# Kernel optimization log

Measured on AMD Instinct MI355X. Metric: run time of the kernel, lower is better.

## Reference

```python
import jax, jax.numpy as jnp
import numpy as np

V, E, NH, NL, FF, MAXLEN = 32000, 512, 8, 4, 2048, 80
B, L = 32, 80
EPS = 1e-5


def _ln(x, w, b):
    m = jnp.mean(x, axis=-1, keepdims=True)
    v = jnp.var(x, axis=-1, keepdims=True)
    return (x - m) / jnp.sqrt(v + EPS) * w + b


def _mha(q_in, kv_in, in_w, in_b, out_w, out_b, mask):
    # in_w: [3E, E] packed q/k/v like torch MultiheadAttention
    Bq, Lq, Em = q_in.shape
    Lk = kv_in.shape[1]
    hd = Em // NH
    q = q_in @ in_w[:Em].T + in_b[:Em]
    k = kv_in @ in_w[Em:2 * Em].T + in_b[Em:2 * Em]
    v = kv_in @ in_w[2 * Em:].T + in_b[2 * Em:]
    q = q.reshape(Bq, Lq, NH, hd).transpose(0, 2, 1, 3)
    k = k.reshape(Bq, Lk, NH, hd).transpose(0, 2, 1, 3)
    v = v.reshape(Bq, Lk, NH, hd).transpose(0, 2, 1, 3)
    s = jnp.einsum('bhqd,bhkd->bhqk', q, k) * (1.0 / float(np.sqrt(hd)))
    if mask is not None:
        s = s + mask
    a = jax.nn.softmax(s, axis=-1)
    o = jnp.einsum('bhqk,bhkd->bhqd', a, v).transpose(0, 2, 1, 3).reshape(Bq, Lq, Em)
    return o @ out_w.T + out_b


def _forward(caps, W_in, b_in, pos_emb, sa_in_w, sa_in_b, sa_out_w, sa_out_b,
             ca_in_w, ca_in_b, ca_out_w, ca_out_b, ff1_w, ff1_b, ff2_w, ff2_b,
             ln1_w, ln1_b, ln2_w, ln2_b, ln3_w, ln3_b, out_w, out_b):
    Bc, Lc = caps.shape
    # one-hot encode then dense Linear(vocab -> emb): semantically an embedding gather
    oh = jax.nn.one_hot(caps, V, dtype=jnp.float32)          # [B, L, V]
    x = oh @ W_in.T + b_in + pos_emb[:Lc][None]               # [B, L, E]
    mask = jnp.where(jnp.triu(jnp.ones((Lc, Lc), bool), 1), -jnp.inf, 0.0).astype(jnp.float32)
    mem = jnp.zeros((Bc, 1, E), jnp.float32)
    for i in range(NL):  # post-norm TransformerDecoderLayer (torch default, relu FFN)
        sa = _mha(x, x, sa_in_w[i], sa_in_b[i], sa_out_w[i], sa_out_b[i], mask)
        x = _ln(x + sa, ln1_w[i], ln1_b[i])
        ca = _mha(x, mem, ca_in_w[i], ca_in_b[i], ca_out_w[i], ca_out_b[i], None)
        x = _ln(x + ca, ln2_w[i], ln2_b[i])
        ff = jax.nn.relu(x @ ff1_w[i].T + ff1_b[i]) @ ff2_w[i].T + ff2_b[i]
        x = _ln(x + ff, ln3_w[i], ln3_b[i])
    return x @ out_w.T + out_b                                # [B, L, V]


def setup_inputs() -> dict:
    key = jax.random.key(0)
    ks = jax.random.split(key, 16)
    g = lambda k, shape, s=0.02: jax.random.normal(k, shape, jnp.float32) * s
    caps = jax.random.randint(ks[0], (B, L), 1, V)  # avoid pad_idx=0
    return {
        'caps': caps,
        'W_in': g(ks[1], (E, V)),
        'b_in': jnp.zeros((E,), jnp.float32),
        'pos_emb': g(ks[2], (MAXLEN, E)),
        'sa_in_w': g(ks[3], (NL, 3 * E, E)),
        'sa_in_b': jnp.zeros((NL, 3 * E), jnp.float32),
        'sa_out_w': g(ks[4], (NL, E, E)),
        'sa_out_b': jnp.zeros((NL, E), jnp.float32),
        'ca_in_w': g(ks[5], (NL, 3 * E, E)),
        'ca_in_b': jnp.zeros((NL, 3 * E), jnp.float32),
        'ca_out_w': g(ks[6], (NL, E, E)),
        'ca_out_b': jnp.zeros((NL, E), jnp.float32),
        'ff1_w': g(ks[7], (NL, FF, E)),
        'ff1_b': jnp.zeros((NL, FF), jnp.float32),
        'ff2_w': g(ks[8], (NL, E, FF)),
        'ff2_b': jnp.zeros((NL, E), jnp.float32),
        'ln1_w': jnp.ones((NL, E), jnp.float32),
        'ln1_b': jnp.zeros((NL, E), jnp.float32),
        'ln2_w': jnp.ones((NL, E), jnp.float32),
        'ln2_b': jnp.zeros((NL, E), jnp.float32),
        'ln3_w': jnp.ones((NL, E), jnp.float32),
        'ln3_b': jnp.zeros((NL, E), jnp.float32),
        'out_w': g(ks[9], (V, E)),
        'out_b': jnp.zeros((V,), jnp.float32),
    }


def reference(caps, W_in, b_in, pos_emb, sa_in_w, sa_in_b, sa_out_w, sa_out_b,
              ca_in_w, ca_in_b, ca_out_w, ca_out_b, ff1_w, ff1_b, ff2_w, ff2_b,
              ln1_w, ln1_b, ln2_w, ln2_b, ln3_w, ln3_b, out_w, out_b):
    return _forward(caps, W_in, b_in, pos_emb, sa_in_w, sa_in_b, sa_out_w, sa_out_b,
                    ca_in_w, ca_in_b, ca_out_w, ca_out_b, ff1_w, ff1_b, ff2_w, ff2_b,
                    ln1_w, ln1_b, ln2_w, ln2_b, ln3_w, ln3_b, out_w, out_b)
```

## Files before the change

kernel.cpp:

```cpp
#include <hip/hip_runtime.h>

typedef __attribute__((ext_vector_type(8))) short short8;
typedef __attribute__((ext_vector_type(4))) float floatx4;

__device__ __forceinline__ unsigned short f2bf(float f) {
  union { float f; unsigned int u; } un; un.f = f;
  unsigned int r = un.u + 0x7FFFu + ((un.u >> 16) & 1u);
  return (unsigned short)(r >> 16);
}
__device__ __forceinline__ float bf2f(unsigned short h) {
  union { unsigned int u; float f; } un; un.u = ((unsigned int)h) << 16;
  return un.f;
}

__device__ __forceinline__ void async_ld16(const unsigned short* g, unsigned short* l) {
  __builtin_amdgcn_global_load_lds(
      (const __attribute__((address_space(1))) void*)g,
      (__attribute__((address_space(3))) void*)l, 16, 0, 0);
}

template<int OUT_BF16, int RELU>
__global__ __launch_bounds__(256, 2)
void gemm_bt(const unsigned short* __restrict__ A, const unsigned short* __restrict__ B,
             const float* __restrict__ bias, const float* __restrict__ res,
             void* __restrict__ Cout, int M, int N, int K) {
  __shared__ __align__(16) unsigned short sA[128 * 64];
  __shared__ __align__(16) unsigned short sB[128 * 64];
  const int tid  = threadIdx.x;
  const int lane = tid & 63;
  const int wave = tid >> 6;
  const int m0 = blockIdx.y * 128;
  const int n0 = blockIdx.x * 128;

  floatx4 acc[4][4];
#pragma unroll
  for (int i = 0; i < 4; i++)
#pragma unroll
    for (int j = 0; j < 4; j++) acc[i][j] = (floatx4){0.f, 0.f, 0.f, 0.f};

  int s_r[4], s_gc[4], s_lb[4];
#pragma unroll
  for (int it = 0; it < 4; it++) {
    int e = it * 2048 + tid * 8;
    int r = e >> 6;
    int cb = (e >> 3) & 7;
    s_r[it]  = r;
    s_gc[it] = (cb ^ (r & 7)) * 8;
    s_lb[it] = it * 2048 + wave * 512;
  }

  const int nkt = K >> 6;
  const int wm = (wave >> 1) * 64;
  const int wn = (wave & 1) * 64;
  const int fr = lane & 15;
  const int q  = lane >> 4;

  for (int kt = 0; kt < nkt; kt++) {
    const int k0 = kt << 6;
#pragma unroll
    for (int it = 0; it < 4; it++) {
      async_ld16(A + (size_t)(m0 + s_r[it]) * K + k0 + s_gc[it], &sA[s_lb[it]]);
      async_ld16(B + (size_t)(n0 + s_r[it]) * K + k0 + s_gc[it], &sB[s_lb[it]]);
    }
    __syncthreads();
#pragma unroll
    for (int kk = 0; kk < 64; kk += 32) {
      short8 af[4], bfr[4];
#pragma unroll
      for (int t = 0; t < 4; t++) {
        int ra = wm + t * 16 + fr;
        int cba = (kk >> 3) + q;
        af[t] = *(const short8*)&sA[ra * 64 + ((cba ^ (ra & 7)) * 8)];
        int rb = wn + t * 16 + fr;
        bfr[t] = *(const short8*)&sB[rb * 64 + ((cba ^ (rb & 7)) * 8)];
      }
#pragma unroll
      for (int i = 0; i < 4; i++)
#pragma unroll
        for (int j = 0; j < 4; j++)
          acc[i][j] = __builtin_amdgcn_mfma_f32_16x16x32_bf16(af[i], bfr[j], acc[i][j], 0, 0, 0);
    }
    __syncthreads();
  }

#pragma unroll
  for (int i = 0; i < 4; i++) {
#pragma unroll
    for (int j = 0; j < 4; j++) {
#pragma unroll
      for (int rg = 0; rg < 4; rg++) {
        int row = m0 + wm + i * 16 + q * 4 + rg;
        int col = n0 + wn + j * 16 + fr;
        float v = acc[i][j][rg];
        if (bias) v += bias[col];
        if (res)  v += res[(size_t)row * N + col];
        if (RELU) v = v > 0.f ? v : 0.f;
        if (OUT_BF16) ((unsigned short*)Cout)[(size_t)row * N + col] = f2bf(v);
        else          ((float*)Cout)[(size_t)row * N + col] = v;
      }
    }
  }
}

__global__ __launch_bounds__(512)
void embed_kernel(const int* __restrict__ caps, const float* __restrict__ W_in,
                  const float* __restrict__ b_in, const float* __restrict__ pos,
                  float* __restrict__ x, unsigned short* __restrict__ xbf) {
  int pidx = blockIdx.x;
  int l = pidx % 80;
  int tok = caps[pidx];
  int e = threadIdx.x;
  float v = W_in[(size_t)e * 32000 + tok] + b_in[e] + pos[l * 512 + e];
  x[(size_t)pidx * 512 + e] = v;
  xbf[(size_t)pidx * 512 + e] = f2bf(v);
}

__global__ __launch_bounds__(256)
void ln_kernel(const float* __restrict__ in, const float* __restrict__ addvec,
               const float* __restrict__ w, const float* __restrict__ b,
               float* __restrict__ xout, unsigned short* __restrict__ xbf) {
  int row = blockIdx.x * 4 + (threadIdx.x >> 6);
  int lane = threadIdx.x & 63;
  const float* p = in + (size_t)row * 512;
  float vals[8];
  float s = 0.f, s2 = 0.f;
#pragma unroll
  for (int j = 0; j < 8; j++) {
    float t = p[lane + j * 64];
    if (addvec) t += addvec[lane + j * 64];
    vals[j] = t; s += t; s2 += t * t;
  }
#pragma unroll
  for (int off = 32; off; off >>= 1) { s += __shfl_xor(s, off); s2 += __shfl_xor(s2, off); }
  float mean = s * (1.f / 512.f);
  float var = s2 * (1.f / 512.f) - mean * mean;
  float inv = rsqrtf(var + 1e-5f);
#pragma unroll
  for (int j = 0; j < 8; j++) {
    int c = lane + j * 64;
    float y = (vals[j] - mean) * inv * w[c] + b[c];
    xout[(size_t)row * 512 + c] = y;
    xbf[(size_t)row * 512 + c] = f2bf(y);
  }
}

__global__ __launch_bounds__(256)
void attn_kernel(const unsigned short* __restrict__ qkv, unsigned short* __restrict__ o) {
  __shared__ unsigned short sq[80][66], sk[80][66], sv[80][66];
  __shared__ float ss[80][81];
  const int tid = threadIdx.x;
  const int bb = blockIdx.x >> 3, hh = blockIdx.x & 7;
  const unsigned short* base = qkv + (size_t)bb * 80 * 1536 + hh * 64;
  for (int idx = tid; idx < 5120; idx += 256) {
    int r = idx >> 6, c = idx & 63;
    sq[r][c] = base[r * 1536 + c];
    sk[r][c] = base[r * 1536 + 512 + c];
    sv[r][c] = base[r * 1536 + 1024 + c];
  }
  __syncthreads();
  {
    const int ti = tid >> 4, tj = tid & 15;
    float acc[5][5];
#pragma unroll
    for (int a = 0; a < 5; a++)
#pragma unroll
      for (int b2 = 0; b2 < 5; b2++) acc[a][b2] = 0.f;
    for (int c = 0; c < 64; c++) {
      float qa[5], kb[5];
#pragma unroll
      for (int a = 0; a < 5; a++) qa[a] = bf2f(sq[ti + a * 16][c]);
#pragma unroll
      for (int b2 = 0; b2 < 5; b2++) kb[b2] = bf2f(sk[tj + b2 * 16][c]);
#pragma unroll
      for (int a = 0; a < 5; a++)
#pragma unroll
        for (int b2 = 0; b2 < 5; b2++) acc[a][b2] += qa[a] * kb[b2];
    }
#pragma unroll
    for (int a = 0; a < 5; a++)
#pragma unroll
      for (int b2 = 0; b2 < 5; b2++) {
        int i = ti + a * 16, j = tj + b2 * 16;
        ss[i][j] = (j <= i) ? acc[a][b2] * 0.125f : -1e30f;
      }
  }
  __syncthreads();
  if (tid < 80) {
    float mx = -1e30f;
    for (int j = 0; j < 80; j++) mx = fmaxf(mx, ss[tid][j]);
    float sum = 0.f;
    for (int j = 0; j < 80; j++) { float e2 = __expf(ss[tid][j] - mx); ss[tid][j] = e2; sum += e2; }
    float inv = 1.f / sum;
    for (int j = 0; j < 80; j++) ss[tid][j] *= inv;
  }
  __syncthreads();
  {
    const int ti = tid >> 4, td = tid & 15;
    float acc[5][4];
#pragma unroll
    for (int a = 0; a < 5; a++)
#pragma unroll
      for (int b2 = 0; b2 < 4; b2++) acc[a][b2] = 0.f;
    for (int j = 0; j < 80; j++) {
      float pa[5], vb[4];
#pragma unroll
      for (int a = 0; a < 5; a++) pa[a] = ss[ti + a * 16][j];
#pragma unroll
      for (int b2 = 0; b2 < 4; b2++) vb[b2] = bf2f(sv[j][td + b2 * 16]);
#pragma unroll
      for (int a = 0; a < 5; a++)
#pragma unroll
        for (int b2 = 0; b2 < 4; b2++) acc[a][b2] += pa[a] * vb[b2];
    }
#pragma unroll
    for (int a = 0; a < 5; a++)
#pragma unroll
      for (int b2 = 0; b2 < 4; b2++) {
        int i = ti + a * 16, d = td + b2 * 16;
        o[((size_t)bb * 80 + i) * 512 + hh * 64 + d] = f2bf(acc[a][b2]);
      }
  }
}

__global__ __launch_bounds__(256)
void cavec_kernel(const float* __restrict__ w, const float* __restrict__ inb,
                  const float* __restrict__ ob, float* __restrict__ out) {
  int e = blockIdx.x * 4 + (threadIdx.x >> 6);
  int lane = threadIdx.x & 63;
  const float* row = w + (size_t)e * 512;
  float s = 0.f;
#pragma unroll
  for (int j = 0; j < 8; j++) s += row[lane + j * 64] * inb[1024 + lane + j * 64];
#pragma unroll
  for (int off = 32; off; off >>= 1) s += __shfl_xor(s, off);
  if (lane == 0) out[e] = s + ob[e];
}

__global__ __launch_bounds__(256)
void convert_f2bf(const float* __restrict__ in, unsigned short* __restrict__ out, int n4) {
  int i = blockIdx.x * 256 + threadIdx.x;
  if (i < n4) {
    float4 v = ((const float4*)in)[i];
    ushort4 r;
    r.x = f2bf(v.x); r.y = f2bf(v.y); r.z = f2bf(v.z); r.w = f2bf(v.w);
    ((ushort4*)out)[i] = r;
  }
}

extern "C" void kernel_launch(void* const* d_in, const int* in_sizes, int n_in,
                              void* d_out, int out_size, void* d_ws, size_t ws_size,
                              hipStream_t stream) {
  const int*   caps     = (const int*)d_in[0];
  const float* W_in     = (const float*)d_in[1];
  const float* b_in     = (const float*)d_in[2];
  const float* pos_emb  = (const float*)d_in[3];
  const float* sa_in_w  = (const float*)d_in[4];
  const float* sa_in_b  = (const float*)d_in[5];
  const float* sa_out_w = (const float*)d_in[6];
  const float* sa_out_b = (const float*)d_in[7];
  const float* ca_in_b  = (const float*)d_in[9];
  const float* ca_out_w = (const float*)d_in[10];
  const float* ca_out_b = (const float*)d_in[11];
  const float* ff1_w    = (const float*)d_in[12];
  const float* ff1_b    = (const float*)d_in[13];
  const float* ff2_w    = (const float*)d_in[14];
  const float* ff2_b    = (const float*)d_in[15];
  const float* ln1_w    = (const float*)d_in[16];
  const float* ln1_b    = (const float*)d_in[17];
  const float* ln2_w    = (const float*)d_in[18];
  const float* ln2_b    = (const float*)d_in[19];
  const float* ln3_w    = (const float*)d_in[20];
  const float* ln3_b    = (const float*)d_in[21];
  const float* out_w    = (const float*)d_in[22];
  const float* out_b    = (const float*)d_in[23];

  char* ws = (char*)d_ws;
  size_t off = 0;
  auto alloc = [&](size_t bytes) {
    void* p = ws + off;
    off += (bytes + 255) & ~(size_t)255;
    return p;
  };
  unsigned short* w_sa_in  = (unsigned short*)alloc((size_t)4 * 1536 * 512 * 2);
  unsigned short* w_sa_out = (unsigned short*)alloc((size_t)4 * 512 * 512 * 2);
  unsigned short* w_ff1    = (unsigned short*)alloc((size_t)4 * 2048 * 512 * 2);
  unsigned short* w_ff2    = (unsigned short*)alloc((size_t)4 * 512 * 2048 * 2);
  unsigned short* w_out    = (unsigned short*)alloc((size_t)32000 * 512 * 2);
  float*          x        = (float*)alloc((size_t)2560 * 512 * 4);
  unsigned short* xbf      = (unsigned short*)alloc((size_t)2560 * 512 * 2);
  float*          t        = (float*)alloc((size_t)2560 * 512 * 4);
  unsigned short* qkv      = (unsigned short*)alloc((size_t)2560 * 1536 * 2);
  unsigned short* obf      = (unsigned short*)alloc((size_t)2560 * 512 * 2);
  unsigned short* hbf      = (unsigned short*)alloc((size_t)2560 * 2048 * 2);
  float*          cav      = (float*)alloc((size_t)512 * 4);

  convert_f2bf<<<(786432 + 255) / 256, 256, 0, stream>>>(sa_in_w, w_sa_in, 786432);
  convert_f2bf<<<(262144 + 255) / 256, 256, 0, stream>>>(sa_out_w, w_sa_out, 262144);
  convert_f2bf<<<(1048576 + 255) / 256, 256, 0, stream>>>(ff1_w, w_ff1, 1048576);
  convert_f2bf<<<(1048576 + 255) / 256, 256, 0, stream>>>(ff2_w, w_ff2, 1048576);
  convert_f2bf<<<(4096000 + 255) / 256, 256, 0, stream>>>(out_w, w_out, 4096000);

  embed_kernel<<<2560, 512, 0, stream>>>(caps, W_in, b_in, pos_emb, x, xbf);

  for (int i = 0; i < 4; i++) {
    gemm_bt<1, 0><<<dim3(12, 20), 256, 0, stream>>>(
        xbf, w_sa_in + (size_t)i * 1536 * 512, sa_in_b + i * 1536, nullptr,
        qkv, 2560, 1536, 512);
    attn_kernel<<<256, 256, 0, stream>>>(qkv, obf);
    gemm_bt<0, 0><<<dim3(4, 20), 256, 0, stream>>>(
        obf, w_sa_out + (size_t)i * 512 * 512, sa_out_b + i * 512, x,
        t, 2560, 512, 512);
    ln_kernel<<<640, 256, 0, stream>>>(t, nullptr, ln1_w + i * 512, ln1_b + i * 512, x, xbf);
    cavec_kernel<<<128, 256, 0, stream>>>(
        ca_out_w + (size_t)i * 512 * 512, ca_in_b + (size_t)i * 1536, ca_out_b + i * 512, cav);
    ln_kernel<<<640, 256, 0, stream>>>(x, cav, ln2_w + i * 512, ln2_b + i * 512, x, xbf);
    gemm_bt<1, 1><<<dim3(16, 20), 256, 0, stream>>>(
        xbf, w_ff1 + (size_t)i * 2048 * 512, ff1_b + i * 2048, nullptr,
        hbf, 2560, 2048, 512);
    gemm_bt<0, 0><<<dim3(4, 20), 256, 0, stream>>>(
        hbf, w_ff2 + (size_t)i * 512 * 2048, ff2_b + i * 512, x,
        t, 2560, 512, 2048);
    ln_kernel<<<640, 256, 0, stream>>>(t, nullptr, ln3_w + i * 512, ln3_b + i * 512, x, xbf);
  }

  gemm_bt<0, 0><<<dim3(250, 20), 256, 0, stream>>>(
      xbf, w_out, out_b, nullptr, (float*)d_out, 2560, 32000, 512);
}
```

Baseline: 1.288 ms.

## Double-buffer GEMM, templatize tiles, MFMA attention, fuse LN1/LN2, hoist cross-attn vector

The GEMM kernel now double-buffers its LDS tiles so the next K-slice's async loads overlap the current MFMAs, and it is templated on tile size. The N=512 GEMMs use 64x64 tiles for more blocks, and the grid is swapped so M varies fastest. Attention computes QK^T and PV with bf16 MFMA instead of scalar FMAs, with V transposed and P rounded to bf16. LN1 and LN2 are fused into one kernel, and the constant cross-attention vector is computed once for all layers before the loop. The costs are doubled LDS use and extra bf16 rounding of the attention probabilities.

```diff
diff --git a/kernel.cpp b/kernel.cpp
--- a/kernel.cpp
+++ b/kernel.cpp
@@ -19,74 +19,92 @@
       (__attribute__((address_space(3))) void*)l, 16, 0, 0);
 }
 
-template<int OUT_BF16, int RELU>
-__global__ __launch_bounds__(256, 2)
+template<int TM, int TN, int OUT_BF16, int RELU>
+__global__ __launch_bounds__(256, (TM == 64) ? 4 : 2)
 void gemm_bt(const unsigned short* __restrict__ A, const unsigned short* __restrict__ B,
              const float* __restrict__ bias, const float* __restrict__ res,
              void* __restrict__ Cout, int M, int N, int K) {
-  __shared__ __align__(16) unsigned short sA[128 * 64];
-  __shared__ __align__(16) unsigned short sB[128 * 64];
-  const int tid  = threadIdx.x;
+  constexpr int AELEM = TM * 64;
+  constexpr int BELEM = TN * 64;
+  constexpr int AIT = AELEM / 2048;
+  constexpr int BIT = BELEM / 2048;
+  constexpr int FM = TM / 32;
+  constexpr int FN = TN / 32;
+  __shared__ __align__(16) unsigned short sA[2][AELEM];
+  __shared__ __align__(16) unsigned short sB[2][BELEM];
+  const int tid = threadIdx.x;
   const int lane = tid & 63;
   const int wave = tid >> 6;
-  const int m0 = blockIdx.y * 128;
-  const int n0 = blockIdx.x * 128;
-
-  floatx4 acc[4][4];
-#pragma unroll
-  for (int i = 0; i < 4; i++)
-#pragma unroll
-    for (int j = 0; j < 4; j++) acc[i][j] = (floatx4){0.f, 0.f, 0.f, 0.f};
-
-  int s_r[4], s_gc[4], s_lb[4];
-#pragma unroll
-  for (int it = 0; it < 4; it++) {
+  const int m0 = blockIdx.x * TM;
+  const int n0 = blockIdx.y * TN;
+
+  int a_off[AIT], b_off[BIT], lb[AIT > BIT ? AIT : BIT];
+#pragma unroll
+  for (int it = 0; it < AIT; it++) {
     int e = it * 2048 + tid * 8;
-    int r = e >> 6;
-    int cb = (e >> 3) & 7;
-    s_r[it]  = r;
-    s_gc[it] = (cb ^ (r & 7)) * 8;
-    s_lb[it] = it * 2048 + wave * 512;
-  }
+    int r = e >> 6, cb = (e >> 3) & 7;
+    a_off[it] = (m0 + r) * K + ((cb ^ (r & 7)) * 8);
+    lb[it] = it * 2048 + wave * 512;
+  }
+#pragma unroll
+  for (int it = 0; it < BIT; it++) {
+    int e = it * 2048 + tid * 8;
+    int r = e >> 6, cb = (e >> 3) & 7;
+    b_off[it] = (n0 + r) * K + ((cb ^ (r & 7)) * 8);
+  }
+
+  floatx4 acc[FM][FN];
+#pragma unroll
+  for (int i = 0; i < FM; i++)
+#pragma unroll
+    for (int j = 0; j < FN; j++) acc[i][j] = (floatx4){0.f, 0.f, 0.f, 0.f};
 
   const int nkt = K >> 6;
-  const int wm = (wave >> 1) * 64;
-  const int wn = (wave & 1) * 64;
+  const int wm = (wave >> 1) * (TM / 2);
+  const int wn = (wave & 1) * (TN / 2);
   const int fr = lane & 15;
-  const int q  = lane >> 4;
-
+  const int q = lane >> 4;
+
+  auto stage = [&](int kt, int buf) {
+    const int k0 = kt << 6;
+#pragma unroll
+    for (int it = 0; it < AIT; it++) async_ld16(A + (size_t)a_off[it] + k0, &sA[buf][lb[it]]);
+#pragma unroll
+    for (int it = 0; it < BIT; it++) async_ld16(B + (size_t)b_off[it] + k0, &sB[buf][lb[it]]);
+  };
+
+  stage(0, 0);
   for (int kt = 0; kt < nkt; kt++) {
-    const int k0 = kt << 6;
-#pragma unroll
-    for (int it = 0; it < 4; it++) {
-      async_ld16(A + (size_t)(m0 + s_r[it]) * K + k0 + s_gc[it], &sA[s_lb[it]]);
-      async_ld16(B + (size_t)(n0 + s_r[it]) * K + k0 + s_gc[it], &sB[s_lb[it]]);
-    }
     __syncthreads();
+    if (kt + 1 < nkt) stage(kt + 1, (kt + 1) & 1);
+    const unsigned short* pA = sA[kt & 1];
+    const unsigned short* pB = sB[kt & 1];
 #pragma unroll
     for (int kk = 0; kk < 64; kk += 32) {
-      short8 af[4], bfr[4];
-#pragma unroll
-      for (int t = 0; t < 4; t++) {
+      short8 af[FM], bfr[FN];
+      const int cba = (kk >> 3) + q;
+#pragma unroll
+      for (int t = 0; t < FM; t++) {
         int ra = wm + t * 16 + fr;
-        int cba = (kk >> 3) + q;
-        af[t] = *(const short8*)&sA[ra * 64 + ((cba ^ (ra & 7)) * 8)];
+        af[t] = *(const short8*)&pA[ra * 64 + ((cba ^ (ra & 7)) * 8)];
+      }
+#pragma unroll
+      for (int t = 0; t < FN; t++) {
         int rb = wn + t * 16 + fr;
-        bfr[t] = *(const short8*)&sB[rb * 64 + ((cba ^ (rb & 7)) * 8)];
+        bfr[t] = *(const short8*)&pB[rb * 64 + ((cba ^ (rb & 7)) * 8)];
       }
 #pragma unroll
-      for (int i = 0; i < 4; i++)
-#pragma unroll
-        for (int j = 0; j < 4; j++)
+      for (int i = 0; i < FM; i++)
+#pragma unroll
+        for (int j = 0; j < FN; j++)
           acc[i][j] = __builtin_amdgcn_mfma_f32_16x16x32_bf16(af[i], bfr[j], acc[i][j], 0, 0, 0);
     }
-    __syncthreads();
-  }
-
-#pragma unroll
-  for (int i = 0; i < 4; i++) {
-#pragma unroll
-    for (int j = 0; j < 4; j++) {
+  }
+
+#pragma unroll
+  for (int i = 0; i < FM; i++) {
+#pragma unroll
+    for (int j = 0; j < FN; j++) {
 #pragma unroll
       for (int rg = 0; rg < 4; rg++) {
         int row = m0 + wm + i * 16 + q * 4 + rg;
@@ -116,9 +134,9 @@
 }
 
 __global__ __launch_bounds__(256)
-void ln_kernel(const float* __restrict__ in, const float* __restrict__ addvec,
-               const float* __restrict__ w, const float* __restrict__ b,
-               float* __restrict__ xout, unsigned short* __restrict__ xbf) {
+void ln_kernel(const float* __restrict__ in, const float* __restrict__ w,
+               const float* __restrict__ b, float* __restrict__ xout,
+               unsigned short* __restrict__ xbf) {
   int row = blockIdx.x * 4 + (threadIdx.x >> 6);
   int lane = threadIdx.x & 63;
   const float* p = in + (size_t)row * 512;
@@ -127,14 +145,12 @@
 #pragma unroll
   for (int j = 0; j < 8; j++) {
     float t = p[lane + j * 64];
-    if (addvec) t += addvec[lane + j * 64];
     vals[j] = t; s += t; s2 += t * t;
   }
 #pragma unroll
   for (int off = 32; off; off >>= 1) { s += __shfl_xor(s, off); s2 += __shfl_xor(s2, off); }
   float mean = s * (1.f / 512.f);
-  float var = s2 * (1.f / 512.f) - mean * mean;
-  float inv = rsqrtf(var + 1e-5f);
+  float inv = rsqrtf(s2 * (1.f / 512.f) - mean * mean + 1e-5f);
 #pragma unroll
   for (int j = 0; j < 8; j++) {
     int c = lane + j * 64;
@@ -145,95 +161,131 @@
 }
 
 __global__ __launch_bounds__(256)
+void ln2x_kernel(const float* __restrict__ in, const float* __restrict__ cav,
+                 const float* __restrict__ w1, const float* __restrict__ b1,
+                 const float* __restrict__ w2, const float* __restrict__ b2,
+                 float* __restrict__ xout, unsigned short* __restrict__ xbf) {
+  int row = blockIdx.x * 4 + (threadIdx.x >> 6);
+  int lane = threadIdx.x & 63;
+  const float* p = in + (size_t)row * 512;
+  float vals[8];
+  float s = 0.f, s2 = 0.f;
+#pragma unroll
+  for (int j = 0; j < 8; j++) {
+    float t = p[lane + j * 64];
+    vals[j] = t; s += t; s2 += t * t;
+  }
+#pragma unroll
+  for (int off = 32; off; off >>= 1) { s += __shfl_xor(s, off); s2 += __shfl_xor(s2, off); }
+  float mean = s * (1.f / 512.f);
+  float inv = rsqrtf(s2 * (1.f / 512.f) - mean * mean + 1e-5f);
+  float s_b = 0.f, s2_b = 0.f;
+#pragma unroll
+  for (int j = 0; j < 8; j++) {
+    int c = lane + j * 64;
+    float y = (vals[j] - mean) * inv * w1[c] + b1[c] + cav[c];
+    vals[j] = y; s_b += y; s2_b += y * y;
+  }
+#pragma unroll
+  for (int off = 32; off; off >>= 1) { s_b += __shfl_xor(s_b, off); s2_b += __shfl_xor(s2_b, off); }
+  float mean2 = s_b * (1.f / 512.f);
+  float inv2 = rsqrtf(s2_b * (1.f / 512.f) - mean2 * mean2 + 1e-5f);
+#pragma unroll
+  for (int j = 0; j < 8; j++) {
+    int c = lane + j * 64;
+    float y = (vals[j] - mean2) * inv2 * w2[c] + b2[c];
+    xout[(size_t)row * 512 + c] = y;
+    xbf[(size_t)row * 512 + c] = f2bf(y);
+  }
+}
+
+__global__ __launch_bounds__(256)
 void attn_kernel(const unsigned short* __restrict__ qkv, unsigned short* __restrict__ o) {
-  __shared__ unsigned short sq[80][66], sk[80][66], sv[80][66];
-  __shared__ float ss[80][81];
+  __shared__ __align__(16) unsigned short sq[80][72];
+  __shared__ __align__(16) unsigned short sk[80][72];
+  __shared__ __align__(16) unsigned short svT[64][96];
+  __shared__ __align__(16) unsigned short sp[80][96];
+  __shared__ float ss[80][84];
   const int tid = threadIdx.x;
+  const int lane = tid & 63;
+  const int wave = tid >> 6;
   const int bb = blockIdx.x >> 3, hh = blockIdx.x & 7;
   const unsigned short* base = qkv + (size_t)bb * 80 * 1536 + hh * 64;
+
   for (int idx = tid; idx < 5120; idx += 256) {
     int r = idx >> 6, c = idx & 63;
     sq[r][c] = base[r * 1536 + c];
     sk[r][c] = base[r * 1536 + 512 + c];
-    sv[r][c] = base[r * 1536 + 1024 + c];
-  }
+    svT[c][r] = base[r * 1536 + 1024 + c];
+  }
+  for (int idx = tid; idx < 1024; idx += 256) svT[idx >> 4][80 + (idx & 15)] = 0;
+  for (int idx = tid; idx < 1280; idx += 256) sp[idx >> 4][80 + (idx & 15)] = 0;
   __syncthreads();
-  {
-    const int ti = tid >> 4, tj = tid & 15;
-    float acc[5][5];
-#pragma unroll
-    for (int a = 0; a < 5; a++)
-#pragma unroll
-      for (int b2 = 0; b2 < 5; b2++) acc[a][b2] = 0.f;
-    for (int c = 0; c < 64; c++) {
-      float qa[5], kb[5];
-#pragma unroll
-      for (int a = 0; a < 5; a++) qa[a] = bf2f(sq[ti + a * 16][c]);
-#pragma unroll
-      for (int b2 = 0; b2 < 5; b2++) kb[b2] = bf2f(sk[tj + b2 * 16][c]);
-#pragma unroll
-      for (int a = 0; a < 5; a++)
-#pragma unroll
-        for (int b2 = 0; b2 < 5; b2++) acc[a][b2] += qa[a] * kb[b2];
-    }
-#pragma unroll
-    for (int a = 0; a < 5; a++)
-#pragma unroll
-      for (int b2 = 0; b2 < 5; b2++) {
-        int i = ti + a * 16, j = tj + b2 * 16;
-        ss[i][j] = (j <= i) ? acc[a][b2] * 0.125f : -1e30f;
-      }
+
+  const int fr = lane & 15;
+  const int q = lane >> 4;
+
+  for (int t = wave; t < 25; t += 4) {
+    int i0 = (t / 5) * 16, j0 = (t % 5) * 16;
+    floatx4 acc = (floatx4){0.f, 0.f, 0.f, 0.f};
+#pragma unroll
+    for (int kk = 0; kk < 64; kk += 32) {
+      short8 a = *(const short8*)&sq[i0 + fr][kk + q * 8];
+      short8 b = *(const short8*)&sk[j0 + fr][kk + q * 8];
+      acc = __builtin_amdgcn_mfma_f32_16x16x32_bf16(a, b, acc, 0, 0, 0);
+    }
+#pragma unroll
+    for (int rg = 0; rg < 4; rg++) {
+      int row = i0 + q * 4 + rg, col = j0 + fr;
+      ss[row][col] = (col <= row) ? acc[rg] * 0.125f : -1e30f;
+    }
   }
   __syncthreads();
+
   if (tid < 80) {
     float mx = -1e30f;
+#pragma unroll
     for (int j = 0; j < 80; j++) mx = fmaxf(mx, ss[tid][j]);
     float sum = 0.f;
-    for (int j = 0; j < 80; j++) { float e2 = __expf(ss[tid][j] - mx); ss[tid][j] = e2; sum += e2; }
+#pragma unroll
+    for (int j = 0; j < 80; j++) { float e = __expf(ss[tid][j] - mx); ss[tid][j] = e; sum += e; }
     float inv = 1.f / sum;
-    for (int j = 0; j < 80; j++) ss[tid][j] *= inv;
+#pragma unroll
+    for (int j = 0; j < 80; j++) sp[tid][j] = f2bf(ss[tid][j] * inv);
   }
   __syncthreads();
-  {
-    const int ti = tid >> 4, td = tid & 15;
-    float acc[5][4];
-#pragma unroll
-    for (int a = 0; a < 5; a++)
-#pragma unroll
-      for (int b2 = 0; b2 < 4; b2++) acc[a][b2] = 0.f;
-    for (int j = 0; j < 80; j++) {
-      float pa[5], vb[4];
-#pragma unroll
-      for (int a = 0; a < 5; a++) pa[a] = ss[ti + a * 16][j];
-#pragma unroll
-      for (int b2 = 0; b2 < 4; b2++) vb[b2] = bf2f(sv[j][td + b2 * 16]);
-#pragma unroll
-      for (int a = 0; a < 5; a++)
-#pragma unroll
-        for (int b2 = 0; b2 < 4; b2++) acc[a][b2] += pa[a] * vb[b2];
-    }
-#pragma unroll
-    for (int a = 0; a < 5; a++)
-#pragma unroll
-      for (int b2 = 0; b2 < 4; b2++) {
-        int i = ti + a * 16, d = td + b2 * 16;
-        o[((size_t)bb * 80 + i) * 512 + hh * 64 + d] = f2bf(acc[a][b2]);
-      }
-  }
-}
-
-__global__ __launch_bounds__(256)
-void cavec_kernel(const float* __restrict__ w, const float* __restrict__ inb,
-                  const float* __restrict__ ob, float* __restrict__ out) {
-  int e = blockIdx.x * 4 + (threadIdx.x >> 6);
+
+  for (int t = wave; t < 20; t += 4) {
+    int i0 = (t / 4) * 16, d0 = (t % 4) * 16;
+    floatx4 acc = (floatx4){0.f, 0.f, 0.f, 0.f};
+#pragma unroll
+    for (int kk = 0; kk < 96; kk += 32) {
+      short8 a = *(const short8*)&sp[i0 + fr][kk + q * 8];
+      short8 b = *(const short8*)&svT[d0 + fr][kk + q * 8];
+      acc = __builtin_amdgcn_mfma_f32_16x16x32_bf16(a, b, acc, 0, 0, 0);
+    }
+#pragma unroll
+    for (int rg = 0; rg < 4; rg++) {
+      int row = i0 + q * 4 + rg;
+      o[((size_t)bb * 80 + row) * 512 + hh * 64 + d0 + fr] = f2bf(acc[rg]);
+    }
+  }
+}
+
+__global__ __launch_bounds__(256)
+void cavec_kernel(const float* __restrict__ ca_out_w, const float* __restrict__ ca_in_b,
+                  const float* __restrict__ ca_out_b, float* __restrict__ cav) {
+  int g = blockIdx.x * 4 + (threadIdx.x >> 6);
   int lane = threadIdx.x & 63;
-  const float* row = w + (size_t)e * 512;
+  int l = g >> 9, e = g & 511;
+  const float* row = ca_out_w + ((size_t)l * 512 + e) * 512;
+  const float* inb = ca_in_b + l * 1536 + 1024;
   float s = 0.f;
 #pragma unroll
-  for (int j = 0; j < 8; j++) s += row[lane + j * 64] * inb[1024 + lane + j * 64];
+  for (int j = 0; j < 8; j++) s += row[lane + j * 64] * inb[lane + j * 64];
 #pragma unroll
   for (int off = 32; off; off >>= 1) s += __shfl_xor(s, off);
-  if (lane == 0) out[e] = s + ob[e];
+  if (lane == 0) cav[g] = s + ca_out_b[l * 512 + e];
 }
 
 __global__ __launch_bounds__(256)
@@ -292,7 +344,7 @@
   unsigned short* qkv      = (unsigned short*)alloc((size_t)2560 * 1536 * 2);
   unsigned short* obf      = (unsigned short*)alloc((size_t)2560 * 512 * 2);
   unsigned short* hbf      = (unsigned short*)alloc((size_t)2560 * 2048 * 2);
-  float*          cav      = (float*)alloc((size_t)512 * 4);
+  float*          cav      = (float*)alloc((size_t)2048 * 4);
 
   convert_f2bf<<<(786432 + 255) / 256, 256, 0, stream>>>(sa_in_w, w_sa_in, 786432);
   convert_f2bf<<<(262144 + 255) / 256, 256, 0, stream>>>(sa_out_w, w_sa_out, 262144);
@@ -301,28 +353,27 @@
   convert_f2bf<<<(4096000 + 255) / 256, 256, 0, stream>>>(out_w, w_out, 4096000);
 
   embed_kernel<<<2560, 512, 0, stream>>>(caps, W_in, b_in, pos_emb, x, xbf);
+  cavec_kernel<<<512, 256, 0, stream>>>(ca_out_w, ca_in_b, ca_out_b, cav);
 
   for (int i = 0; i < 4; i++) {
-    gemm_bt<1, 0><<<dim3(12, 20), 256, 0, stream>>>(
+    gemm_bt<128, 128, 1, 0><<<dim3(20, 12), 256, 0, stream>>>(
         xbf, w_sa_in + (size_t)i * 1536 * 512, sa_in_b + i * 1536, nullptr,
         qkv, 2560, 1536, 512);
     attn_kernel<<<256, 256, 0, stream>>>(qkv, obf);
-    gemm_bt<0, 0><<<dim3(4, 20), 256, 0, stream>>>(
+    gemm_bt<64, 64, 0, 0><<<dim3(40, 8), 256, 0, stream>>>(
         obf, w_sa_out + (size_t)i * 512 * 512, sa_out_b + i * 512, x,
         t, 2560, 512, 512);
-    ln_kernel<<<640, 256, 0, stream>>>(t, nullptr, ln1_w + i * 512, ln1_b + i * 512, x, xbf);
-    cavec_kernel<<<128, 256, 0, stream>>>(
-        ca_out_w + (size_t)i * 512 * 512, ca_in_b + (size_t)i * 1536, ca_out_b + i * 512, cav);
-    ln_kernel<<<640, 256, 0, stream>>>(x, cav, ln2_w + i * 512, ln2_b + i * 512, x, xbf);
-    gemm_bt<1, 1><<<dim3(16, 20), 256, 0, stream>>>(
+    ln2x_kernel<<<640, 256, 0, stream>>>(t, cav + i * 512,
+        ln1_w + i * 512, ln1_b + i * 512, ln2_w + i * 512, ln2_b + i * 512, x, xbf);
+    gemm_bt<128, 128, 1, 1><<<dim3(20, 16), 256, 0, stream>>>(
         xbf, w_ff1 + (size_t)i * 2048 * 512, ff1_b + i * 2048, nullptr,
         hbf, 2560, 2048, 512);
-    gemm_bt<0, 0><<<dim3(4, 20), 256, 0, stream>>>(
+    gemm_bt<64, 64, 0, 0><<<dim3(40, 8), 256, 0, stream>>>(
         hbf, w_ff2 + (size_t)i * 512 * 2048, ff2_b + i * 512, x,
         t, 2560, 512, 2048);
-    ln_kernel<<<640, 256, 0, stream>>>(t, nullptr, ln3_w + i * 512, ln3_b + i * 512, x, xbf);
-  }
-
-  gemm_bt<0, 0><<<dim3(250, 20), 256, 0, stream>>>(
+    ln_kernel<<<640, 256, 0, stream>>>(t, ln3_w + i * 512, ln3_b + i * 512, x, xbf);
+  }
+
+  gemm_bt<128, 128, 0, 0><<<dim3(20, 250), 256, 0, stream>>>(
       xbf, w_out, out_b, nullptr, (float*)d_out, 2560, 32000, 512);
 }
```

Result: faster. 1.121 ms (-13.0%).
